# Performance work log

Measured on AMD Instinct MI355X. Metric: run time of the kernel, lower is better.

Reference implementation:

```python
import jax, jax.numpy as jnp
import numpy as np

P = 20000          # plan nodes (queries)
H = 128            # hidden_dim_plan
DIMS = {"table": (100000, 96), "pred": (400000, 160), "agg": (60000, 64), "join": (80000, 64)}
BN_EPS = 1e-5


def setup_inputs() -> dict:
    key = jax.random.key(0)
    ks = iter(jax.random.split(key, 32))
    inp = {}
    for t, (n, d) in DIMS.items():
        inp[f"feat_{t}"] = jax.random.normal(next(ks), (n, d), dtype=jnp.float32)
        inp[f"idx_{t}"] = jax.random.randint(next(ks), (n,), 0, P)
        # per-type encoder: Linear(d, H) (stored as [d, H])
        inp[f"W_{t}"] = jax.random.normal(next(ks), (d, H), dtype=jnp.float32) * 0.02
        inp[f"b_{t}"] = jnp.zeros((H,), jnp.float32)
    # est head: BatchNorm1d(4H) -> Linear(4H,H)+ReLU -> Linear(H,H)+ReLU -> Linear(H,1)
    inp["bn_gamma"] = jnp.ones((4 * H,), jnp.float32)
    inp["bn_beta"] = jnp.zeros((4 * H,), jnp.float32)
    inp["W1"] = jax.random.normal(next(ks), (4 * H, H), dtype=jnp.float32) * 0.02
    inp["b1"] = jnp.zeros((H,), jnp.float32)
    inp["W2"] = jax.random.normal(next(ks), (H, H), dtype=jnp.float32) * 0.02
    inp["b2"] = jnp.zeros((H,), jnp.float32)
    inp["W3"] = jax.random.normal(next(ks), (H, 1), dtype=jnp.float32) * 0.02
    inp["b3"] = jnp.zeros((1,), jnp.float32)
    inp["num_plan"] = P
    return inp


def _seg_mean(x, idx, num_seg):
    # DGL mean pooling: mean over incoming edges, 0 for nodes with no edges
    s = jax.ops.segment_sum(x, idx, num_segments=num_seg)
    c = jax.ops.segment_sum(jnp.ones((x.shape[0], 1), x.dtype), idx, num_segments=num_seg)
    return s / jnp.maximum(c, 1.0)


def _forward(feats, idxs, params, num_plan):
    pooled = []
    for t in ("table", "pred", "agg", "join"):
        enc = jax.nn.relu(feats[t] @ params[f"W_{t}"] + params[f"b_{t}"])  # [N_t, H]
        pooled.append(_seg_mean(enc, idxs[t], num_plan))                    # [P, H]
    x = jnp.concatenate(pooled, axis=1)  # [P, 4H]
    # BatchNorm1d (training mode: batch statistics, biased variance)
    mu = jnp.mean(x, axis=0)
    var = jnp.mean(jnp.square(x - mu), axis=0)
    x = (x - mu) * jax.lax.rsqrt(var + BN_EPS) * params["bn_gamma"] + params["bn_beta"]
    x = jax.nn.relu(x @ params["W1"] + params["b1"])
    x = jax.nn.relu(x @ params["W2"] + params["b2"])
    return x @ params["W3"] + params["b3"]  # [P, 1]


def reference(feat_table, feat_pred, feat_agg, feat_join,
              W_table, b_table, W_pred, b_pred, W_agg, b_agg, W_join, b_join,
              bn_gamma, bn_beta, W1, b1, W2, b2, W3, b3,
              idx_table, idx_pred, idx_agg, idx_join, num_plan):
    feats = {"table": feat_table, "pred": feat_pred, "agg": feat_agg, "join": feat_join}
    idxs = {"table": idx_table, "pred": idx_pred, "agg": idx_agg, "join": idx_join}
    params = dict(W_table=W_table, b_table=b_table, W_pred=W_pred, b_pred=b_pred,
                  W_agg=W_agg, b_agg=b_agg, W_join=W_join, b_join=b_join,
                  bn_gamma=bn_gamma, bn_beta=bn_beta, W1=W1, b1=b1, W2=W2, b2=b2, W3=W3, b3=b3)
    return _forward(feats, idxs, params, num_plan)
```

## Files before the change

### kernel.cpp

```cpp
#include <hip/hip_runtime.h>
#include <cstdint>


constexpr int P_N = 20000;
constexpr int HD  = 128;

typedef __attribute__((ext_vector_type(8))) short  short8v;
typedef __attribute__((ext_vector_type(4))) float  float4v;
typedef __attribute__((ext_vector_type(8))) float  float8v;
typedef __attribute__((ext_vector_type(8))) __bf16 bf16x8;

__device__ inline ushort f2bf(float f) {
    uint32_t u = __builtin_bit_cast(uint32_t, f);
    u += 0x7fffu + ((u >> 16) & 1u);
    return (ushort)(u >> 16);
}
__device__ inline short8v cvt8v(float4 a, float4 b) {
    float8v f = {a.x, a.y, a.z, a.w, b.x, b.y, b.z, b.w};
    bf16x8 h = __builtin_convertvector(f, bf16x8);
    return __builtin_bit_cast(short8v, h);
}
__device__ inline float4v mfma16(short8v a, short8v b, float4v c) {
    return __builtin_amdgcn_mfma_f32_16x16x32_bf16(a, b, c, 0, 0, 0);
}

__global__ void k_count_zero(const int* __restrict__ i0, const int* __restrict__ i1,
                             const int* __restrict__ i2, const int* __restrict__ i3,
                             int n0, int n1, int n2, int n3, int* __restrict__ counts,
                             int nb_count, float4* __restrict__ xz) {
    if (blockIdx.x < (unsigned)nb_count) {
        int i = blockIdx.x * blockDim.x + threadIdx.x;
        const int n01 = n0 + n1, n012 = n0 + n1 + n2, tot = n012 + n3;
        if (i >= tot) return;
        int tp, li; const int* p;
        if (i < n0)        { tp = 0; li = i;        p = i0; }
        else if (i < n01)  { tp = 1; li = i - n0;   p = i1; }
        else if (i < n012) { tp = 2; li = i - n01;  p = i2; }
        else               { tp = 3; li = i - n012; p = i3; }
        atomicAdd(&counts[tp * P_N + p[li]], 1);
    } else {
        const int NZ = P_N * 128;
        int i = (blockIdx.x - nb_count) * blockDim.x + threadIdx.x;
        const int stride = 2048 * 256;
        const float4 z = {0.f, 0.f, 0.f, 0.f};
        for (; i < NZ; i += stride) xz[i] = z;
    }
}

__global__ void k_scan(int* __restrict__ counts_all, int* __restrict__ cur_all,
                       float* __restrict__ invc,
                       int* l0, int* l1, int* l2, int* l3,
                       int* s0, int* s1, int* s2, int* s3,
                       int n0, int n1, int n2, int n3) {
    const int type = blockIdx.x;
    int* counts = counts_all + type * P_N;
    int* curs   = cur_all   + type * P_N;
    float* ic   = invc      + type * P_N;
    const int T = 256;
    const int CH = (P_N + T - 1) / T;
    int t = threadIdx.x;
    __shared__ int sums[T];
    __shared__ int pref[T];
    int local = 0;
    int p0 = t * CH;
    for (int i = 0; i < CH; ++i) {
        int p = p0 + i;
        if (p < P_N) local += counts[p];
    }
    sums[t] = local;
    __syncthreads();
    if (t == 0) {
        int run = 0;
        for (int j = 0; j < T; ++j) { pref[j] = run; run += sums[j]; }
    }
    __syncthreads();
    int run = pref[t];
    for (int i = 0; i < CH; ++i) {
        int p = p0 + i;
        if (p < P_N) {
            int c = counts[p];
            curs[p] = run; run += c;
            ic[p] = 1.f / (float)max(c, 1);
        }
    }
    int N; int *lp, *sp;
    if (type == 0)      { N = n0; lp = l0; sp = s0; }
    else if (type == 1) { N = n1; lp = l1; sp = s1; }
    else if (type == 2) { N = n2; lp = l2; sp = s2; }
    else                { N = n3; lp = l3; sp = s3; }
    if (t < 160) { lp[N + t] = 0; sp[N + t] = -1; }
}

__global__ void k_fill_prepw(const int* __restrict__ i0, const int* __restrict__ i1,
                             const int* __restrict__ i2, const int* __restrict__ i3,
                             int n0, int n1, int n2, int n3, int* __restrict__ cur_all,
                             int* l0, int* l1, int* l2, int* l3,
                             int* s0p, int* s1p, int* s2p, int* s3p,
                             int nb_fill,
                             const float* w0s, const float* w1s, const float* w2s,
                             const float* w3s, const float* w4s, const float* w5s,
                             ushort* d0, ushort* d1, ushort* d2, ushort* d3,
                             ushort* d4, ushort* d5) {
    if (blockIdx.x < (unsigned)nb_fill) {
        int i = blockIdx.x * blockDim.x + threadIdx.x;
        const int n01 = n0 + n1, n012 = n0 + n1 + n2, tot = n012 + n3;
        if (i >= tot) return;
        int tp, li; const int* p; int *lst, *spl;
        if (i < n0)        { tp = 0; li = i;        p = i0; lst = l0; spl = s0p; }
        else if (i < n01)  { tp = 1; li = i - n0;   p = i1; lst = l1; spl = s1p; }
        else if (i < n012) { tp = 2; li = i - n01;  p = i2; lst = l2; spl = s2p; }
        else               { tp = 3; li = i - n012; p = i3; lst = l3; spl = s3p; }
        int pl = p[li];
        int pos = atomicAdd(&cur_all[tp * P_N + pl], 1);
        lst[pos] = li;
        spl[pos] = pl;
    } else {
        int i = (blockIdx.x - nb_fill) * blockDim.x + threadIdx.x;
        const float* s; ushort* d; int Dv, li;
        if (i < 12288)       { s = w0s; d = d0; Dv = 96;  li = i; }
        else if (i < 32768)  { s = w1s; d = d1; Dv = 160; li = i - 12288; }
        else if (i < 40960)  { s = w2s; d = d2; Dv = 64;  li = i - 32768; }
        else if (i < 49152)  { s = w3s; d = d3; Dv = 64;  li = i - 40960; }
        else if (i < 114688) { s = w4s; d = d4; Dv = 512; li = i - 49152; }
        else if (i < 131072) { s = w5s; d = d5; Dv = 128; li = i - 114688; }
        else return;
        int n = li / Dv, k = li - n * Dv;
        d[li] = f2bf(s[k * HD + n]);
    }
}

__device__ __forceinline__ void reduce_group(float (*Cs)[132], const int* plans,
                                             float* __restrict__ x, int toff, int pbase) {
    const int t = threadIdx.x;
    const int col = t & 127, half = t >> 7;
    int curp = -2; float s = 0.f;
    #pragma unroll 8
    for (int r = 0; r < 32; ++r) {
        int p = plans[pbase + half * 32 + r];
        float v = Cs[half * 32 + r][col];
        if (p != curp) {
            if (curp >= 0) atomicAdd(&x[(size_t)curp * 512 + toff + col], s);
            s = 0.f; curp = p;
        }
        if (p >= 0) s += v;
    }
    if (curp >= 0) atomicAdd(&x[(size_t)curp * 512 + toff + col], s);
}

template<int D>
__device__ __forceinline__ void enc_body(
    const float* __restrict__ feat, const ushort* __restrict__ WT,
    const float* __restrict__ bias, const int* __restrict__ list,
    const int* __restrict__ splan, float* __restrict__ x, int toff, int tile,
    float (*Cs)[132], int* plans)
{
    constexpr int NKS = D / 32;
    const int t = threadIdx.x;
    const int w = t >> 6, lane = t & 63;
    const int lq = lane >> 4, lr = lane & 15;
    const int m0 = tile * 128;

    if (t < 128) plans[t] = splan[m0 + t];
    const int l0v = list[m0 + w * 16 + lr];
    const int l1v = list[m0 + 64 + w * 16 + lr];

    const float* a0p = feat + (size_t)l0v * D + lq * 8;
    const float* a1p = feat + (size_t)l1v * D + lq * 8;

    float4 s0[2 * NKS], s1[2 * NKS];
    #pragma unroll
    for (int ks = 0; ks < NKS; ++ks) {
        s0[2 * ks]     = *(const float4*)(a0p + ks * 32);
        s0[2 * ks + 1] = *(const float4*)(a0p + ks * 32 + 4);
    }
    #pragma unroll
    for (int ks = 0; ks < NKS; ++ks) {
        s1[2 * ks]     = *(const float4*)(a1p + ks * 32);
        s1[2 * ks + 1] = *(const float4*)(a1p + ks * 32 + 4);
    }
    short8v a0[NKS], a1[NKS];
    #pragma unroll
    for (int ks = 0; ks < NKS; ++ks) a0[ks] = cvt8v(s0[2 * ks], s0[2 * ks + 1]);
    #pragma unroll
    for (int ks = 0; ks < NKS; ++ks) a1[ks] = cvt8v(s1[2 * ks], s1[2 * ks + 1]);

    float bv[8];
    #pragma unroll
    for (int nf = 0; nf < 8; ++nf) bv[nf] = bias[nf * 16 + lr];

    float4v acc0[8], acc1[8];
    #pragma unroll
    for (int nf = 0; nf < 8; ++nf) {
        acc0[nf] = (float4v){0.f, 0.f, 0.f, 0.f};
        acc1[nf] = (float4v){0.f, 0.f, 0.f, 0.f};
    }

    const ushort* wp = WT + lr * D + lq * 8;
    short8v bcur[8];
    #pragma unroll
    for (int nf = 0; nf < 8; ++nf) bcur[nf] = *(const short8v*)(wp + nf * 16 * D);
    #pragma unroll
    for (int ks = 0; ks < NKS; ++ks) {
        short8v bnxt[8];
        if (ks + 1 < NKS) {
            #pragma unroll
            for (int nf = 0; nf < 8; ++nf)
                bnxt[nf] = *(const short8v*)(wp + nf * 16 * D + (ks + 1) * 32);
        }
        #pragma unroll
        for (int nf = 0; nf < 8; ++nf) acc0[nf] = mfma16(a0[ks], bcur[nf], acc0[nf]);
        #pragma unroll
        for (int nf = 0; nf < 8; ++nf) acc1[nf] = mfma16(a1[ks], bcur[nf], acc1[nf]);
        if (ks + 1 < NKS) {
            #pragma unroll
            for (int nf = 0; nf < 8; ++nf) bcur[nf] = bnxt[nf];
        }
    }

    #pragma unroll
    for (int nf = 0; nf < 8; ++nf) {
        #pragma unroll
        for (int j = 0; j < 4; ++j)
            Cs[w * 16 + lq * 4 + j][nf * 16 + lr] = fmaxf(acc0[nf][j] + bv[nf], 0.f);
    }
    __syncthreads();
    reduce_group(Cs, plans, x, toff, 0);
    __syncthreads();
    #pragma unroll
    for (int nf = 0; nf < 8; ++nf) {
        #pragma unroll
        for (int j = 0; j < 4; ++j)
            Cs[w * 16 + lq * 4 + j][nf * 16 + lr] = fmaxf(acc1[nf][j] + bv[nf], 0.f);
    }
    __syncthreads();
    reduce_group(Cs, plans, x, toff, 64);
}

__global__ __launch_bounds__(256, 2) void k_enc_all(
    const float* f0, const float* f1, const float* f2, const float* f3,
    const ushort* w0, const ushort* w1, const ushort* w2, const ushort* w3,
    const float* b0, const float* b1, const float* b2, const float* b3,
    const int* l0, const int* l1, const int* l2, const int* l3,
    const int* s0, const int* s1, const int* s2, const int* s3,
    float* x, int ntp, int ntt, int nta)
{
    __shared__ float Cs[64][132];
    __shared__ int plans[128];
    int bid = blockIdx.x;
    if (bid < ntp) { enc_body<160>(f1, w1, b1, l1, s1, x, 128, bid, Cs, plans); return; }
    bid -= ntp;
    if (bid < ntt) { enc_body<96>(f0, w0, b0, l0, s0, x, 0, bid, Cs, plans); return; }
    bid -= ntt;
    if (bid < nta) { enc_body<64>(f2, w2, b2, l2, s2, x, 256, bid, Cs, plans); return; }
    bid -= nta;
    enc_body<64>(f3, w3, b3, l3, s3, x, 384, bid, Cs, plans);
}

__global__ __launch_bounds__(512) void k_bnstats(
    const float* __restrict__ x, const float* __restrict__ invc,
    float* __restrict__ bnsum, int* __restrict__ done,
    const float* __restrict__ gamma, const float* __restrict__ beta,
    float* __restrict__ scale, float* __restrict__ shiftv)
{
    const int t = threadIdx.x;
    const int r0 = blockIdx.x * 40;
    const int r1 = min(r0 + 40, P_N);
    const float* ic = invc + (t >> 7) * P_N;
    float s = 0.f, q = 0.f;
    for (int r = r0; r < r1; ++r) {
        float v = x[(size_t)r * 512 + t] * ic[r];
        s += v; q += v * v;
    }
    atomicAdd(&bnsum[t], s);
    atomicAdd(&bnsum[512 + t], q);

    __shared__ int amLast;
    __syncthreads();
    if (t == 0) {
        __threadfence();
        int prev = __hip_atomic_fetch_add(done, 1, __ATOMIC_ACQ_REL, __HIP_MEMORY_SCOPE_AGENT);
        amLast = (prev == (int)gridDim.x - 1);
    }
    __syncthreads();
    if (amLast) {
        const float invn = 1.f / (float)P_N;
        float sm = __hip_atomic_load(&bnsum[t],       __ATOMIC_RELAXED, __HIP_MEMORY_SCOPE_AGENT);
        float sq = __hip_atomic_load(&bnsum[512 + t], __ATOMIC_RELAXED, __HIP_MEMORY_SCOPE_AGENT);
        float mu  = sm * invn;
        float var = sq * invn - mu * mu;
        float rstd = rsqrtf(fmaxf(var, 0.f) + 1e-5f);
        float sc = gamma[t] * rstd;
        scale[t]  = sc;
        shiftv[t] = beta[t] - mu * sc;
    }
}

__global__ __launch_bounds__(256) void k_head(
    const float* __restrict__ x, const float* __restrict__ invc,
    const float* __restrict__ scale, const float* __restrict__ shiftv,
    const ushort* __restrict__ WT1, const float* __restrict__ b1,
    const ushort* __restrict__ WT2, const float* __restrict__ b2,
    const float* __restrict__ W3, const float* __restrict__ b3,
    float* __restrict__ out)
{
    __shared__ float h[16][132];
    __shared__ float red[4][16];
    const int t = threadIdx.x;
    const int w = t >> 6, lane = t & 63;
    const int lq = lane >> 4, lr = lane & 15;
    const int p0 = blockIdx.x * 16;
    const int row = p0 + lr;
    const float* xr = x + (size_t)row * 512;

    float4v acc[2];
    #pragma unroll
    for (int nf = 0; nf < 2; ++nf) acc[nf] = (float4v){0.f, 0.f, 0.f, 0.f};

    #pragma unroll
    for (int kc = 0; kc < 4; ++kc) {
        const float ic = invc[kc * P_N + row];
        float4 st[8];
        #pragma unroll
        for (int k2 = 0; k2 < 4; ++k2) {
            const int k0 = kc * 128 + k2 * 32 + lq * 8;
            st[2 * k2]     = *(const float4*)(xr + k0);
            st[2 * k2 + 1] = *(const float4*)(xr + k0 + 4);
        }
        short8v a[4];
        #pragma unroll
        for (int k2 = 0; k2 < 4; ++k2) {
            const int k0 = kc * 128 + k2 * 32 + lq * 8;
            float4 sc0 = *(const float4*)(scale + k0);
            float4 sc1 = *(const float4*)(scale + k0 + 4);
            float4 sh0 = *(const float4*)(shiftv + k0);
            float4 sh1 = *(const float4*)(shiftv + k0 + 4);
            float4 v0, v1;
            v0.x = st[2*k2].x   * ic * sc0.x + sh0.x;
            v0.y = st[2*k2].y   * ic * sc0.y + sh0.y;
            v0.z = st[2*k2].z   * ic * sc0.z + sh0.z;
            v0.w = st[2*k2].w   * ic * sc0.w + sh0.w;
            v1.x = st[2*k2+1].x * ic * sc1.x + sh1.x;
            v1.y = st[2*k2+1].y * ic * sc1.y + sh1.y;
            v1.z = st[2*k2+1].z * ic * sc1.z + sh1.z;
            v1.w = st[2*k2+1].w * ic * sc1.w + sh1.w;
            a[k2] = cvt8v(v0, v1);
        }
        #pragma unroll
        for (int k2 = 0; k2 < 4; ++k2) {
            const int ks = kc * 4 + k2;
            #pragma unroll
            for (int nf = 0; nf < 2; ++nf) {
                short8v b = *(const short8v*)(WT1 + (size_t)(w * 32 + nf * 16 + lr) * 512 + ks * 32 + lq * 8);
                acc[nf] = mfma16(a[k2], b, acc[nf]);
            }
        }
    }
    #pragma unroll
    for (int nf = 0; nf < 2; ++nf) {
        const int c = w * 32 + nf * 16 + lr;
        const float bvv = b1[c];
        #pragma unroll
        for (int j = 0; j < 4; ++j)
            h[lq * 4 + j][c] = fmaxf(acc[nf][j] + bvv, 0.f);
    }
    __syncthreads();

    short8v a2[4];
    #pragma unroll
    for (int ks = 0; ks < 4; ++ks) {
        const float* hp = &h[lr][ks * 32 + lq * 8];
        a2[ks] = cvt8v(*(const float4*)hp, *(const float4*)(hp + 4));
    }
    float4v acc2[2];
    #pragma unroll
    for (int nf = 0; nf < 2; ++nf) acc2[nf] = (float4v){0.f, 0.f, 0.f, 0.f};
    #pragma unroll
    for (int ks = 0; ks < 4; ++ks) {
        #pragma unroll
        for (int nf = 0; nf < 2; ++nf) {
            short8v b = *(const short8v*)(WT2 + (w * 32 + nf * 16 + lr) * 128 + ks * 32 + lq * 8);
            acc2[nf] = mfma16(a2[ks], b, acc2[nf]);
        }
    }

    float s0 = 0.f, s1 = 0.f, s2 = 0.f, s3 = 0.f;
    #pragma unroll
    for (int nf = 0; nf < 2; ++nf) {
        const int c = w * 32 + nf * 16 + lr;
        const float w3v = W3[c];
        const float bvv = b2[c];
        s0 += fmaxf(acc2[nf][0] + bvv, 0.f) * w3v;
        s1 += fmaxf(acc2[nf][1] + bvv, 0.f) * w3v;
        s2 += fmaxf(acc2[nf][2] + bvv, 0.f) * w3v;
        s3 += fmaxf(acc2[nf][3] + bvv, 0.f) * w3v;
    }
    #pragma unroll
    for (int o = 1; o < 16; o <<= 1) {
        s0 += __shfl_xor(s0, o);
        s1 += __shfl_xor(s1, o);
        s2 += __shfl_xor(s2, o);
        s3 += __shfl_xor(s3, o);
    }
    if (lr == 0) {
        red[w][lq * 4 + 0] = s0;
        red[w][lq * 4 + 1] = s1;
        red[w][lq * 4 + 2] = s2;
        red[w][lq * 4 + 3] = s3;
    }
    __syncthreads();
    if (t < 16) out[p0 + t] = red[0][t] + red[1][t] + red[2][t] + red[3][t] + b3[0];
}

extern "C" void kernel_launch(void* const* d_in, const int* in_sizes, int n_in,
                              void* d_out, int out_size, void* d_ws, size_t ws_size,
                              hipStream_t stream)
{
    const float* feats[4] = {(const float*)d_in[0], (const float*)d_in[4], (const float*)d_in[8],  (const float*)d_in[12]};
    const int*   idxs[4]  = {(const int*)d_in[1],   (const int*)d_in[5],   (const int*)d_in[9],   (const int*)d_in[13]};
    const float* Ws[4]    = {(const float*)d_in[2], (const float*)d_in[6], (const float*)d_in[10], (const float*)d_in[14]};
    const float* bs[4]    = {(const float*)d_in[3], (const float*)d_in[7], (const float*)d_in[11], (const float*)d_in[15]};
    const float* gamma = (const float*)d_in[16];
    const float* beta  = (const float*)d_in[17];
    const float* W1 = (const float*)d_in[18]; const float* b1 = (const float*)d_in[19];
    const float* W2 = (const float*)d_in[20]; const float* b2 = (const float*)d_in[21];
    const float* W3 = (const float*)d_in[22]; const float* b3 = (const float*)d_in[23];
    int Ns[4] = {in_sizes[1], in_sizes[5], in_sizes[9], in_sizes[13]};

    char* ws = (char*)d_ws;
    int*   counts = (int*)(ws + 0);
    float* bnsum  = (float*)(ws + 320000);
    int*   done   = (int*)(ws + 324096);
    float* x      = (float*)(ws + 324352);
    int*   curs   = (int*)(ws + 41284352);
    int* lists[4];
    lists[0] = (int*)(ws + 41604352);
    lists[1] = (int*)(ws + 42004992);
    lists[2] = (int*)(ws + 43605632);
    lists[3] = (int*)(ws + 43846272);
    int* splans[4];
    splans[0] = (int*)(ws + 44166912);
    splans[1] = (int*)(ws + 44567552);
    splans[2] = (int*)(ws + 46168192);
    splans[3] = (int*)(ws + 46408832);
    ushort* WTs[4];
    WTs[0] = (ushort*)(ws + 46729472);
    WTs[1] = (ushort*)(ws + 46754048);
    WTs[2] = (ushort*)(ws + 46795008);
    WTs[3] = (ushort*)(ws + 46811392);
    float* invc   = (float*)(ws + 46827776);
    ushort* WT1   = (ushort*)(ws + 47147776);
    ushort* WT2   = (ushort*)(ws + 47278848);
    float* scale  = (float*)(ws + 47311616);
    float* shiftv = (float*)(ws + 47313664);

    hipMemsetAsync(ws, 0, 324352, stream);

    const int tot = Ns[0] + Ns[1] + Ns[2] + Ns[3];
    const int nb_count = (tot + 255) / 256;
    k_count_zero<<<nb_count + 2048, 256, 0, stream>>>(
        idxs[0], idxs[1], idxs[2], idxs[3], Ns[0], Ns[1], Ns[2], Ns[3], counts,
        nb_count, (float4*)x);
    k_scan<<<4, 256, 0, stream>>>(counts, curs, invc,
        lists[0], lists[1], lists[2], lists[3],
        splans[0], splans[1], splans[2], splans[3],
        Ns[0], Ns[1], Ns[2], Ns[3]);
    const int nb_fill = (tot + 255) / 256;
    k_fill_prepw<<<nb_fill + 512, 256, 0, stream>>>(
        idxs[0], idxs[1], idxs[2], idxs[3], Ns[0], Ns[1], Ns[2], Ns[3], curs,
        lists[0], lists[1], lists[2], lists[3],
        splans[0], splans[1], splans[2], splans[3],
        nb_fill,
        Ws[0], Ws[1], Ws[2], Ws[3], W1, W2,
        WTs[0], WTs[1], WTs[2], WTs[3], WT1, WT2);
    const int ntp = (Ns[1] + 127) / 128, ntt = (Ns[0] + 127) / 128;
    const int nta = (Ns[2] + 127) / 128, ntj = (Ns[3] + 127) / 128;
    k_enc_all<<<ntp + ntt + nta + ntj, 256, 0, stream>>>(
        feats[0], feats[1], feats[2], feats[3],
        WTs[0], WTs[1], WTs[2], WTs[3],
        bs[0], bs[1], bs[2], bs[3],
        lists[0], lists[1], lists[2], lists[3],
        splans[0], splans[1], splans[2], splans[3],
        x, ntp, ntt, nta);
    k_bnstats<<<500, 512, 0, stream>>>(x, invc, bnsum, done, gamma, beta, scale, shiftv);
    k_head<<<P_N / 16, 256, 0, stream>>>(x, invc, scale, shiftv,
                                         WT1, b1, WT2, b2, W3, b3, (float*)d_out);
}
```

Baseline: 384.0 us.

## Split encoder tile across 8 waves, one 16-row fragment per wave

After: 400.8 us. 1.04x slower.

```diff
diff --git a/kernel.cpp b/kernel.cpp
--- a/kernel.cpp
+++ b/kernel.cpp
@@ -132,6 +132,7 @@
 __device__ __forceinline__ void reduce_group(float (*Cs)[132], const int* plans,
                                              float* __restrict__ x, int toff, int pbase) {
     const int t = threadIdx.x;
+    if (t >= 256) return;
     const int col = t & 127, half = t >> 7;
     int curp = -2; float s = 0.f;
     #pragma unroll 8
@@ -161,82 +162,61 @@
     const int m0 = tile * 128;
 
     if (t < 128) plans[t] = splan[m0 + t];
-    const int l0v = list[m0 + w * 16 + lr];
-    const int l1v = list[m0 + 64 + w * 16 + lr];
-
-    const float* a0p = feat + (size_t)l0v * D + lq * 8;
-    const float* a1p = feat + (size_t)l1v * D + lq * 8;
-
-    float4 s0[2 * NKS], s1[2 * NKS];
+    const int lv = list[m0 + w * 16 + lr];
+    const float* ap = feat + (size_t)lv * D + lq * 8;
+
+    float4 st[2 * NKS];
     #pragma unroll
     for (int ks = 0; ks < NKS; ++ks) {
-        s0[2 * ks]     = *(const float4*)(a0p + ks * 32);
-        s0[2 * ks + 1] = *(const float4*)(a0p + ks * 32 + 4);
-    }
+        st[2 * ks]     = *(const float4*)(ap + ks * 32);
+        st[2 * ks + 1] = *(const float4*)(ap + ks * 32 + 4);
+    }
+    short8v a[NKS];
+    #pragma unroll
+    for (int ks = 0; ks < NKS; ++ks) a[ks] = cvt8v(st[2 * ks], st[2 * ks + 1]);
+
+    float bv[8];
+    #pragma unroll
+    for (int nf = 0; nf < 8; ++nf) bv[nf] = bias[nf * 16 + lr];
+
+    float4v acc[8];
+    #pragma unroll
+    for (int nf = 0; nf < 8; ++nf) acc[nf] = (float4v){0.f, 0.f, 0.f, 0.f};
+
+    const ushort* wp = WT + lr * D + lq * 8;
     #pragma unroll
     for (int ks = 0; ks < NKS; ++ks) {
-        s1[2 * ks]     = *(const float4*)(a1p + ks * 32);
-        s1[2 * ks + 1] = *(const float4*)(a1p + ks * 32 + 4);
-    }
-    short8v a0[NKS], a1[NKS];
-    #pragma unroll
-    for (int ks = 0; ks < NKS; ++ks) a0[ks] = cvt8v(s0[2 * ks], s0[2 * ks + 1]);
-    #pragma unroll
-    for (int ks = 0; ks < NKS; ++ks) a1[ks] = cvt8v(s1[2 * ks], s1[2 * ks + 1]);
-
-    float bv[8];
-    #pragma unroll
-    for (int nf = 0; nf < 8; ++nf) bv[nf] = bias[nf * 16 + lr];
-
-    float4v acc0[8], acc1[8];
-    #pragma unroll
-    for (int nf = 0; nf < 8; ++nf) {
-        acc0[nf] = (float4v){0.f, 0.f, 0.f, 0.f};
-        acc1[nf] = (float4v){0.f, 0.f, 0.f, 0.f};
-    }
-
-    const ushort* wp = WT + lr * D + lq * 8;
-    short8v bcur[8];
-    #pragma unroll
-    for (int nf = 0; nf < 8; ++nf) bcur[nf] = *(const short8v*)(wp + nf * 16 * D);
-    #pragma unroll
-    for (int ks = 0; ks < NKS; ++ks) {
-        short8v bnxt[8];
-        if (ks + 1 < NKS) {
+        #pragma unroll
+        for (int nf = 0; nf < 8; ++nf) {
+            short8v b = *(const short8v*)(wp + nf * 16 * D + ks * 32);
+            acc[nf] = mfma16(a[ks], b, acc[nf]);
+        }
+    }
+
+    if (w < 4) {
+        #pragma unroll
+        for (int nf = 0; nf < 8; ++nf) {
             #pragma unroll
-            for (int nf = 0; nf < 8; ++nf)
-                bnxt[nf] = *(const short8v*)(wp + nf * 16 * D + (ks + 1) * 32);
-        }
-        #pragma unroll
-        for (int nf = 0; nf < 8; ++nf) acc0[nf] = mfma16(a0[ks], bcur[nf], acc0[nf]);
-        #pragma unroll
-        for (int nf = 0; nf < 8; ++nf) acc1[nf] = mfma16(a1[ks], bcur[nf], acc1[nf]);
-        if (ks + 1 < NKS) {
+            for (int j = 0; j < 4; ++j)
+                Cs[w * 16 + lq * 4 + j][nf * 16 + lr] = fmaxf(acc[nf][j] + bv[nf], 0.f);
+        }
+    }
+    __syncthreads();
+    reduce_group(Cs, plans, x, toff, 0);
+    __syncthreads();
+    if (w >= 4) {
+        #pragma unroll
+        for (int nf = 0; nf < 8; ++nf) {
             #pragma unroll
-            for (int nf = 0; nf < 8; ++nf) bcur[nf] = bnxt[nf];
-        }
-    }
-
-    #pragma unroll
-    for (int nf = 0; nf < 8; ++nf) {
-        #pragma unroll
-        for (int j = 0; j < 4; ++j)
-            Cs[w * 16 + lq * 4 + j][nf * 16 + lr] = fmaxf(acc0[nf][j] + bv[nf], 0.f);
-    }
-    __syncthreads();
-    reduce_group(Cs, plans, x, toff, 0);
-    __syncthreads();
-    #pragma unroll
-    for (int nf = 0; nf < 8; ++nf) {
-        #pragma unroll
-        for (int j = 0; j < 4; ++j)
-            Cs[w * 16 + lq * 4 + j][nf * 16 + lr] = fmaxf(acc1[nf][j] + bv[nf], 0.f);
+            for (int j = 0; j < 4; ++j)
+                Cs[(w - 4) * 16 + lq * 4 + j][nf * 16 + lr] = fmaxf(acc[nf][j] + bv[nf], 0.f);
+        }
     }
     __syncthreads();
     reduce_group(Cs, plans, x, toff, 64);
 }
 
-__global__ __launch_bounds__(256, 2) void k_enc_all(
+__global__ __launch_bounds__(512, 2) void k_enc_all(
     const float* f0, const float* f1, const float* f2, const float* f3,
     const ushort* w0, const ushort* w1, const ushort* w2, const ushort* w3,
     const float* b0, const float* b1, const float* b2, const float* b3,
@@ -474,7 +454,7 @@
         WTs[0], WTs[1], WTs[2], WTs[3], WT1, WT2);
     const int ntp = (Ns[1] + 127) / 128, ntt = (Ns[0] + 127) / 128;
     const int nta = (Ns[2] + 127) / 128, ntj = (Ns[3] + 127) / 128;
-    k_enc_all<<<ntp + ntt + nta + ntj, 256, 0, stream>>>(
+    k_enc_all<<<ntp + ntt + nta + ntj, 512, 0, stream>>>(
         feats[0], feats[1], feats[2], feats[3],
         WTs[0], WTs[1], WTs[2], WTs[3],
         bs[0], bs[1], bs[2], bs[3],
```
